# Kernel optimization log

Measured on AMD Instinct MI355X. Metric: run time of the kernel, lower is better.

## Reference

```python
import jax, jax.numpy as jnp
import numpy as np

B, T, D, H = 2, 2048, 1024, 16
DH = D // H  # 64


def setup_inputs() -> dict:
    key = jax.random.key(0)
    ks = jax.random.split(key, 8)
    s = 0.02  # typical init scale for projection weights
    return {
        "query_states": jax.random.normal(ks[0], (B, T, D), jnp.float32),
        "key_states": jax.random.normal(ks[1], (B, T, D), jnp.float32),
        "attention_mask": jnp.zeros((B, 1, 1, T), jnp.float32),
        "Wq": jax.random.normal(ks[2], (D, D), jnp.float32) * s,
        "bq": jnp.zeros((D,), jnp.float32),
        "Wk": jax.random.normal(ks[3], (D, D), jnp.float32) * s,
        "bk": jnp.zeros((D,), jnp.float32),
        "Wv": jax.random.normal(ks[4], (D, D), jnp.float32) * s,
        "bv": jnp.zeros((D,), jnp.float32),
        "mask_future": 0,
    }


def _heads(x):
    # [B, T, D] -> [B, H, T, DH]
    b, t, _ = x.shape
    return x.reshape(b, t, H, DH).transpose(0, 2, 1, 3)


def reference(query_states, key_states, attention_mask, Wq, bq, Wk, bk, Wv, bv, mask_future):
    q = _heads(query_states @ Wq + bq)   # [B,H,T,DH]
    k = _heads(key_states @ Wk + bk)     # [B,H,T,DH]
    v = _heads(key_states @ Wv + bv)     # [B,H,T,DH]
    scale = 1.0 / jnp.sqrt(jnp.asarray(DH, jnp.float32))
    scores = jnp.einsum("bhqd,bhkd->bhqk", q, k) * scale + attention_mask
    if mask_future:  # static Python int flag
        t = scores.shape[-1]
        triu = jnp.triu(jnp.ones((t, t), bool))  # includes diagonal, as in torch.triu
        scores = jnp.where(triu, -jnp.inf, scores)
    probs = jax.nn.softmax(scores, axis=-1)
    # dropout p=0.0 -> identity
    ctx = jnp.einsum("bhqk,bhkd->bhqd", probs, v)  # [B,H,T,DH]
    b, _, t, _ = ctx.shape
    return ctx.transpose(0, 2, 1, 3).reshape(b, t, H * DH)
```

## Files before the change

kernel.cpp:

```cpp
#include <hip/hip_runtime.h>

#define DEV __device__ __forceinline__

typedef _Float16 f16;
typedef __attribute__((ext_vector_type(2))) _Float16 f16x2;
typedef __attribute__((ext_vector_type(4))) _Float16 f16x4;
typedef __attribute__((ext_vector_type(8))) _Float16 f16x8;
typedef __attribute__((ext_vector_type(4))) float f32x4;
typedef __attribute__((ext_vector_type(16))) float f32x16;
typedef __attribute__((ext_vector_type(4))) int i32x4;

constexpr int B = 2, T = 2048, D = 1024, H = 16, DH = 64;
constexpr int M = B * T;
constexpr float LOG2E = 1.4426950408889634f;

DEV void gload_lds16(const void* g, void* l) {
  __builtin_amdgcn_global_load_lds(
      (const __attribute__((address_space(1))) void*)g,
      (__attribute__((address_space(3))) void*)l, 16, 0, 0);
}

DEV unsigned pack_pk(float a, float b) {
  auto v = __builtin_amdgcn_cvt_pkrtz(a, b);
  return __builtin_bit_cast(unsigned, v);
}

DEV float max3f(float a, float b, float c) { return fmaxf(fmaxf(a, b), c); }

#if __has_builtin(__builtin_amdgcn_permlane32_swap)
#define HAVE_PLSWAP 1
DEV void swap32(unsigned& a, unsigned& b) {
  auto r = __builtin_amdgcn_permlane32_swap((int)a, (int)b, false, false);
  a = (unsigned)r[0];
  b = (unsigned)r[1];
}
DEV float redmax32(float x) {
  unsigned a = __builtin_bit_cast(unsigned, x), b = a;
  swap32(a, b);
  return fmaxf(__builtin_bit_cast(float, a), __builtin_bit_cast(float, b));
}
DEV float redsum32(float x) {
  unsigned a = __builtin_bit_cast(unsigned, x), b = a;
  swap32(a, b);
  return __builtin_bit_cast(float, a) + __builtin_bit_cast(float, b);
}
#else
#define HAVE_PLSWAP 0
DEV float redmax32(float x) { return fmaxf(x, __shfl_xor(x, 32, 64)); }
DEV float redsum32(float x) { return x + __shfl_xor(x, 32, 64); }
#endif

__global__ __launch_bounds__(256) void cast_qk(
    const float* __restrict__ qin, const float* __restrict__ kin,
    f16* __restrict__ outq) {
  int bi = blockIdx.x;
  const float* in = (bi < 2048) ? qin : kin;
  f16* out = outq + ((bi < 2048) ? 0 : (size_t)M * D);
  int i = ((bi & 2047) * 256 + threadIdx.x) * 8;
  f32x4 a = *(const f32x4*)(in + i);
  f32x4 b = *(const f32x4*)(in + i + 4);
  f16x8 o;
  o[0] = (f16)a[0]; o[1] = (f16)a[1]; o[2] = (f16)a[2]; o[3] = (f16)a[3];
  o[4] = (f16)b[0]; o[5] = (f16)b[1]; o[6] = (f16)b[2]; o[7] = (f16)b[3];
  *(f16x8*)(out + i) = o;
}

__global__ __launch_bounds__(256) void transpose_cast(
    const float* __restrict__ Wq, const float* __restrict__ Wk,
    const float* __restrict__ Wv, f16* __restrict__ WT) {
  int mat = blockIdx.z;
  const float* W = (mat == 0) ? Wq : (mat == 1 ? Wk : Wv);
  f16* out = WT + (size_t)mat * D * D;
  __shared__ float tile[32][33];
  int nt = blockIdx.x * 32, kt = blockIdx.y * 32;
  int tx = threadIdx.x, ty = threadIdx.y;
  for (int j = 0; j < 4; ++j) {
    int r = ty + 8 * j;
    tile[r][tx] = W[(size_t)(kt + r) * D + nt + tx];
  }
  __syncthreads();
  for (int j = 0; j < 4; ++j) {
    int r = ty + 8 * j;
    out[(size_t)(nt + r) * D + kt + tx] = (f16)tile[tx][r];
  }
}

__global__ __launch_bounds__(256) void qkv_gemm(
    const f16* __restrict__ XQ, const f16* __restrict__ XK,
    const f16* __restrict__ WT, const float* __restrict__ bq,
    const float* __restrict__ bk, const float* __restrict__ bv,
    f16* __restrict__ QKV) {
  int mat = blockIdx.z;
  const f16* X = (mat == 0) ? XQ : XK;
  const f16* Wt = WT + (size_t)mat * D * D;
  const float* bias = (mat == 0) ? bq : (mat == 1 ? bk : bv);
  f16* out = QKV + (size_t)mat * M * D;
  float oscale = (mat == 0) ? 0.125f * LOG2E : 1.0f;
  int Lb = blockIdx.x + 8 * blockIdx.y;
  int n0 = (Lb & 7) * 128, m0 = (Lb >> 3) * 128;

  __shared__ f16 lds[2 * 2 * 128 * 64];
  char* lAb = (char*)lds;
  char* lBb = (char*)lds + 16384;

  int tid = threadIdx.x;
  int w = tid >> 6, lane = tid & 63;
  int l15 = lane & 15, lhi = lane >> 4;
  int wr = w >> 1, wc = w & 1;
  int r8 = lane >> 3, slot = lane & 7;
  int sslot = slot ^ r8;

  f32x4 acc[4][4] = {};
  constexpr int NKT = D / 64;

  auto STAGE = [&](int kt, int buf) {
#pragma unroll
    for (int i = 0; i < 4; ++i) {
      int chunk = w * 4 + i;
      int row = chunk * 8 + r8;
      gload_lds16(X + (size_t)(m0 + row) * D + kt * 64 + sslot * 8,
                  lAb + buf * 32768 + chunk * 1024);
      gload_lds16(Wt + (size_t)(n0 + row) * D + kt * 64 + sslot * 8,
                  lBb + buf * 32768 + chunk * 1024);
    }
  };

  STAGE(0, 0);
  __syncthreads();

  for (int kt = 0; kt < NKT; ++kt) {
    if (kt) __syncthreads();
    if (kt + 1 < NKT) STAGE(kt + 1, (kt + 1) & 1);
    const char* bA = lAb + (kt & 1) * 32768;
    const char* bB = lBb + (kt & 1) * 32768;
#pragma unroll
    for (int ks = 0; ks < 2; ++ks) {
      f16x8 aF[4], bF[4];
#pragma unroll
      for (int mt = 0; mt < 4; ++mt) {
        int row = wr * 64 + mt * 16 + l15;
        int byt = (row * 128 + ks * 64 + lhi * 16) ^ ((row & 7) << 4);
        aF[mt] = *(const f16x8*)(bA + byt);
      }
#pragma unroll
      for (int nt = 0; nt < 4; ++nt) {
        int row = wc * 64 + nt * 16 + l15;
        int byt = (row * 128 + ks * 64 + lhi * 16) ^ ((row & 7) << 4);
        bF[nt] = *(const f16x8*)(bB + byt);
      }
      __builtin_amdgcn_s_setprio(1);
#pragma unroll
      for (int mt = 0; mt < 4; ++mt)
#pragma unroll
        for (int nt = 0; nt < 4; ++nt)
          acc[mt][nt] = __builtin_amdgcn_mfma_f32_16x16x32_f16(
              aF[mt], bF[nt], acc[mt][nt], 0, 0, 0);
      __builtin_amdgcn_s_setprio(0);
    }
  }

  float bv4[4];
  for (int nt = 0; nt < 4; ++nt) bv4[nt] = bias[n0 + wc * 64 + nt * 16 + l15];
  if (mat < 2) {
    for (int mt = 0; mt < 4; ++mt)
      for (int nt = 0; nt < 4; ++nt) {
        int col = n0 + wc * 64 + nt * 16 + l15;
        int hh = col >> 6, dh = col & 63;
        for (int r = 0; r < 4; ++r) {
          int row = m0 + wr * 64 + mt * 16 + lhi * 4 + r;
          int bb = row >> 11, tt = row & (T - 1);
          out[((size_t)(bb * H + hh) * T + tt) * 64 + dh] =
              (f16)((acc[mt][nt][r] + bv4[nt]) * oscale);
        }
      }
  } else {
    for (int mt = 0; mt < 4; ++mt)
      for (int nt = 0; nt < 4; ++nt) {
        int col = n0 + wc * 64 + nt * 16 + l15;
        int hh = col >> 6, dh = col & 63;
        int row0 = m0 + wr * 64 + mt * 16 + lhi * 4;
        int bb = row0 >> 11, tt = row0 & (T - 1);
        f16x4 pk;
        for (int r = 0; r < 4; ++r) pk[r] = (f16)(acc[mt][nt][r] + bv4[nt]);
        *(f16x4*)(out + ((size_t)(bb * H + hh) * 64 + dh) * T + tt) = pk;
      }
  }
}

__global__ __launch_bounds__(256) void attn(
    const f16* __restrict__ QKV, const float* __restrict__ mask,
    const int* __restrict__ mfp, float* __restrict__ out) {
  int L = blockIdx.x + 16 * blockIdx.y + 256 * blockIdx.z;
  int e = L & 7, q = L >> 3;
  int bh = e * 4 + (q & 3);
  int q0 = (q >> 2) * 128;
  int b = bh >> 4, h = bh & 15;
  int mf = *mfp;
  constexpr int NT = T / 64;

  const f16* Qh = QKV + (size_t)bh * T * 64;
  const f16* Kh = QKV + (size_t)M * D + (size_t)bh * T * 64;
  const f16* VTh = QKV + (size_t)2 * M * D + (size_t)bh * 64 * T;

  __shared__ char smem[32768];

  int tid = threadIdx.x;
  int w = tid >> 6, lane = tid & 63;
  int l31 = lane & 31, hi = lane >> 5;
  int qrow = q0 + w * 32 + l31;

  const float* mb = mask + (size_t)b * T;
  bool lnz = false;
#pragma unroll
  for (int j = 0; j < 8; ++j) {
    f32x4 mv = *(const f32x4*)(mb + lane * 32 + j * 4);
    lnz |= (mv[0] != 0.f) | (mv[1] != 0.f) | (mv[2] != 0.f) | (mv[3] != 0.f);
  }
  int domask = __any(lnz) | mf;

  f16x8 qF[4];
  const f16* qp = Qh + (size_t)qrow * 64;
#pragma unroll
  for (int kc = 0; kc < 4; ++kc) qF[kc] = *(const f16x8*)(qp + kc * 16 + hi * 8);

  auto STAGE = [&](int kv0, int buf) {
    char* dK = smem + buf * 8192;
    char* dV = smem + 16384 + buf * 8192;
#pragma unroll
    for (int i = 0; i < 2; ++i) {
      int c = (w * 2 + i) * 64 + lane;
      int r = c >> 3;
      int slot = (c & 7) ^ (r & 7);
      gload_lds16(Kh + (size_t)(kv0 + r) * 64 + slot * 8, dK + (w * 2 + i) * 1024);
      gload_lds16(VTh + (size_t)r * T + kv0 + slot * 8, dV + (w * 2 + i) * 1024);
    }
  };

  float mprev = -1e30f, lsum = 0.f;
  f32x16 oAcc[2] = {};
  STAGE(0, 0);
  __syncthreads();

  for (int t = 0; t < NT; ++t) {
    if (t) __syncthreads();
    if (t + 1 < NT) STAGE((t + 1) * 64, (t + 1) & 1);
    int kv0 = t * 64;
    const char* bK = smem + (t & 1) * 8192;
    const char* bV = smem + 16384 + (t & 1) * 8192;

    f32x16 sA[2] = {};
    __builtin_amdgcn_s_setprio(1);
#pragma unroll
    for (int f = 0; f < 2; ++f)
#pragma unroll
      for (int kc = 0; kc < 4; ++kc) {
        int row = f * 32 + l31;
        f16x8 kF = *(const f16x8*)(bK + ((row * 128 + kc * 32 + hi * 16) ^ ((row & 7) << 4)));
        sA[f] = __builtin_amdgcn_mfma_f32_32x32x16_f16(kF, qF[kc], sA[f], 0, 0, 0);
      }
    __builtin_amdgcn_s_setprio(0);

    float mx;
    if (domask) {
      mx = -1e30f;
#pragma unroll
      for (int f = 0; f < 2; ++f)
#pragma unroll
        for (int r = 0; r < 16; ++r) {
          int kv = kv0 + f * 32 + (r & 3) + 8 * (r >> 2) + 4 * hi;
          float v = sA[f][r] + LOG2E * mb[kv];
          if (mf && kv >= qrow) v = -1e30f;
          sA[f][r] = v;
          mx = fmaxf(mx, v);
        }
    } else {
      float t0 = max3f(sA[0][0], sA[0][1], sA[0][2]);
      float t1 = max3f(sA[0][3], sA[0][4], sA[0][5]);
      float t2 = max3f(sA[0][6], sA[0][7], sA[0][8]);
      float t3 = max3f(sA[0][9], sA[0][10], sA[0][11]);
      float t4 = max3f(sA[0][12], sA[0][13], sA[0][14]);
      float t5 = max3f(sA[1][0], sA[1][1], sA[1][2]);
      float t6 = max3f(sA[1][3], sA[1][4], sA[1][5]);
      float t7 = max3f(sA[1][6], sA[1][7], sA[1][8]);
      float t8 = max3f(sA[1][9], sA[1][10], sA[1][11]);
      float t9 = max3f(sA[1][12], sA[1][13], sA[1][14]);
      float u0 = max3f(t0, t1, t2);
      float u1 = max3f(t3, t4, sA[0][15]);
      float u2 = max3f(t5, t6, t7);
      float u3 = max3f(t8, t9, sA[1][15]);
      mx = fmaxf(max3f(u0, u1, u2), u3);
    }
    mx = redmax32(mx);

    if (!__all(mx <= mprev + 8.f)) {
      float mn = fmaxf(mprev, mx);
      float asc = __builtin_amdgcn_exp2f(mprev - mn);
      lsum *= asc;
#pragma unroll
      for (int f = 0; f < 2; ++f)
#pragma unroll
        for (int r = 0; r < 16; ++r) oAcc[f][r] *= asc;
      mprev = mn;
    }

    float rs = 0.f;
#pragma unroll
    for (int f = 0; f < 2; ++f)
#pragma unroll
      for (int r = 0; r < 16; ++r) {
        float e2 = __builtin_amdgcn_exp2f(sA[f][r] - mprev);
        sA[f][r] = e2;
        rs += e2;
      }
    lsum += redsum32(rs);

    f16x8 pF[4];
#if HAVE_PLSWAP
#pragma unroll
    for (int f = 0; f < 2; ++f)
#pragma unroll
      for (int half = 0; half < 2; ++half) {
        unsigned p0 = pack_pk(sA[f][half * 8 + 0], sA[f][half * 8 + 1]);
        unsigned p1 = pack_pk(sA[f][half * 8 + 2], sA[f][half * 8 + 3]);
        unsigned p2 = pack_pk(sA[f][half * 8 + 4], sA[f][half * 8 + 5]);
        unsigned p3 = pack_pk(sA[f][half * 8 + 6], sA[f][half * 8 + 7]);
        swap32(p0, p2);
        swap32(p1, p3);
        i32x4 d;
        d[0] = (int)p0; d[1] = (int)p1; d[2] = (int)p2; d[3] = (int)p3;
        pF[f * 2 + half] = __builtin_bit_cast(f16x8, d);
      }
#else
#pragma unroll
    for (int f = 0; f < 2; ++f) {
      unsigned pk_[8], px_[8];
#pragma unroll
      for (int g = 0; g < 8; ++g) {
        pk_[g] = pack_pk(sA[f][2 * g], sA[f][2 * g + 1]);
        px_[g] = (unsigned)__shfl_xor((int)pk_[g], 32, 64);
      }
#pragma unroll
      for (int half = 0; half < 2; ++half) {
        int o = half * 4;
        i32x4 d;
        d[0] = (int)(hi ? px_[o + 2] : pk_[o + 0]);
        d[1] = (int)(hi ? px_[o + 3] : pk_[o + 1]);
        d[2] = (int)(hi ? pk_[o + 2] : px_[o + 0]);
        d[3] = (int)(hi ? pk_[o + 3] : px_[o + 1]);
        pF[f * 2 + half] = __builtin_bit_cast(f16x8, d);
      }
    }
#endif

    __builtin_amdgcn_s_setprio(1);
#pragma unroll
    for (int df = 0; df < 2; ++df)
#pragma unroll
      for (int kc = 0; kc < 4; ++kc) {
        int row = df * 32 + l31;
        f16x8 vF = *(const f16x8*)(bV + ((row * 128 + kc * 32 + hi * 16) ^ ((row & 7) << 4)));
        oAcc[df] = __builtin_amdgcn_mfma_f32_32x32x16_f16(vF, pF[kc], oAcc[df], 0, 0, 0);
      }
    __builtin_amdgcn_s_setprio(0);
  }

  __syncthreads();
  float linv = 1.0f / lsum;
  float* sOw = (float*)smem + w * 2048;
#pragma unroll
  for (int df = 0; df < 2; ++df)
#pragma unroll
    for (int r = 0; r < 16; ++r) {
      int d = df * 32 + 4 * hi + (r & 3) + 8 * (r >> 2);
      sOw[l31 * 64 + (d ^ l31)] = oAcc[df][r] * linv;
    }
  __syncthreads();
  float* op0 = out + (size_t)(b * T + q0 + w * 32) * D + h * 64;
#pragma unroll
  for (int r2 = 0; r2 < 32; ++r2) {
    float v = sOw[r2 * 64 + (lane ^ r2)];
    op0[(size_t)r2 * D + lane] = v;
  }
}

extern "C" void kernel_launch(void* const* d_in, const int* in_sizes, int n_in,
                              void* d_out, int out_size, void* d_ws, size_t ws_size,
                              hipStream_t stream) {
  const float* q_in = (const float*)d_in[0];
  const float* k_in = (const float*)d_in[1];
  const float* amask = (const float*)d_in[2];
  const float* Wq = (const float*)d_in[3];
  const float* bq = (const float*)d_in[4];
  const float* Wk = (const float*)d_in[5];
  const float* bk = (const float*)d_in[6];
  const float* Wv = (const float*)d_in[7];
  const float* bv = (const float*)d_in[8];
  const int* mf = (const int*)d_in[9];
  float* out = (float*)d_out;

  char* ws = (char*)d_ws;
  f16* XQK = (f16*)ws;
  f16* WT = (f16*)(ws + (((size_t)16) << 20));
  f16* QKV = (f16*)(ws + (((size_t)24) << 20));

  cast_qk<<<4096, 256, 0, stream>>>(q_in, k_in, XQK);
  transpose_cast<<<dim3(32, 32, 3), dim3(32, 8), 0, stream>>>(Wq, Wk, Wv, WT);
  qkv_gemm<<<dim3(8, 32, 3), 256, 0, stream>>>(XQK, XQK + (size_t)M * D, WT, bq,
                                               bk, bv, QKV);
  attn<<<dim3(16, 16, 2), 256, 0, stream>>>(QKV, amask, mf, out);
}
```

Measured before the change: 203.5 us.

## Merge prep kernels, single-buffer QKV GEMM, stage epilogue through LDS

Combines the input cast and weight transpose-cast into one launch to save a kernel launch. The QKV GEMM drops double-buffered LDS prefetch and setprio in favour of a single buffer with two barriers per k-step. Its epilogue now writes results to swizzled LDS and then emits coalesced 16-byte global stores for both the head-major Q/K layout and the transposed V layout. The attention softmax row sum is now a tree reduction over the exponentiated scores instead of a serial accumulation. Removing the prefetch exposes global load latency in the GEMM main loop, which may offset the cheaper epilogue.

Result: no change. 207.0 us (+1.7%).

```diff
diff --git a/kernel.cpp b/kernel.cpp
--- a/kernel.cpp
+++ b/kernel.cpp
@@ -27,6 +27,14 @@
 
 DEV float max3f(float a, float b, float c) { return fmaxf(fmaxf(a, b), c); }
 
+DEV float sum16(const f32x16& v) {
+  float a = (v[0] + v[1]) + (v[2] + v[3]);
+  float b = (v[4] + v[5]) + (v[6] + v[7]);
+  float c = (v[8] + v[9]) + (v[10] + v[11]);
+  float d = (v[12] + v[13]) + (v[14] + v[15]);
+  return (a + b) + (c + d);
+}
+
 #if __has_builtin(__builtin_amdgcn_permlane32_swap)
 #define HAVE_PLSWAP 1
 DEV void swap32(unsigned& a, unsigned& b) {
@@ -50,30 +58,33 @@
 DEV float redsum32(float x) { return x + __shfl_xor(x, 32, 64); }
 #endif
 
-__global__ __launch_bounds__(256) void cast_qk(
+__global__ __launch_bounds__(256) void prep(
     const float* __restrict__ qin, const float* __restrict__ kin,
-    f16* __restrict__ outq) {
+    const float* __restrict__ Wq, const float* __restrict__ Wk,
+    const float* __restrict__ Wv, f16* __restrict__ XQK,
+    f16* __restrict__ WT) {
   int bi = blockIdx.x;
-  const float* in = (bi < 2048) ? qin : kin;
-  f16* out = outq + ((bi < 2048) ? 0 : (size_t)M * D);
-  int i = ((bi & 2047) * 256 + threadIdx.x) * 8;
-  f32x4 a = *(const f32x4*)(in + i);
-  f32x4 b = *(const f32x4*)(in + i + 4);
-  f16x8 o;
-  o[0] = (f16)a[0]; o[1] = (f16)a[1]; o[2] = (f16)a[2]; o[3] = (f16)a[3];
-  o[4] = (f16)b[0]; o[5] = (f16)b[1]; o[6] = (f16)b[2]; o[7] = (f16)b[3];
-  *(f16x8*)(out + i) = o;
-}
-
-__global__ __launch_bounds__(256) void transpose_cast(
-    const float* __restrict__ Wq, const float* __restrict__ Wk,
-    const float* __restrict__ Wv, f16* __restrict__ WT) {
-  int mat = blockIdx.z;
+  int tid = threadIdx.x;
+  if (bi < 4096) {
+    const float* in = (bi < 2048) ? qin : kin;
+    f16* out = XQK + ((bi < 2048) ? 0 : (size_t)M * D);
+    int i = ((bi & 2047) * 256 + tid) * 8;
+    f32x4 a = *(const f32x4*)(in + i);
+    f32x4 b = *(const f32x4*)(in + i + 4);
+    f16x8 o;
+    o[0] = (f16)a[0]; o[1] = (f16)a[1]; o[2] = (f16)a[2]; o[3] = (f16)a[3];
+    o[4] = (f16)b[0]; o[5] = (f16)b[1]; o[6] = (f16)b[2]; o[7] = (f16)b[3];
+    *(f16x8*)(out + i) = o;
+    return;
+  }
+  int t = bi - 4096;
+  int mat = t >> 10;
+  int rem = t & 1023;
+  int nt = (rem & 31) * 32, kt = (rem >> 5) * 32;
   const float* W = (mat == 0) ? Wq : (mat == 1 ? Wk : Wv);
   f16* out = WT + (size_t)mat * D * D;
   __shared__ float tile[32][33];
-  int nt = blockIdx.x * 32, kt = blockIdx.y * 32;
-  int tx = threadIdx.x, ty = threadIdx.y;
+  int tx = tid & 31, ty = tid >> 5;
   for (int j = 0; j < 4; ++j) {
     int r = ty + 8 * j;
     tile[r][tx] = W[(size_t)(kt + r) * D + nt + tx];
@@ -99,7 +110,7 @@
   int Lb = blockIdx.x + 8 * blockIdx.y;
   int n0 = (Lb & 7) * 128, m0 = (Lb >> 3) * 128;
 
-  __shared__ f16 lds[2 * 2 * 128 * 64];
+  __shared__ f16 lds[2 * 128 * 64];
   char* lAb = (char*)lds;
   char* lBb = (char*)lds + 16384;
 
@@ -111,28 +122,19 @@
   int sslot = slot ^ r8;
 
   f32x4 acc[4][4] = {};
-  constexpr int NKT = D / 64;
-
-  auto STAGE = [&](int kt, int buf) {
+
+  for (int kt = 0; kt < D / 64; ++kt) {
+    __syncthreads();
 #pragma unroll
     for (int i = 0; i < 4; ++i) {
       int chunk = w * 4 + i;
       int row = chunk * 8 + r8;
       gload_lds16(X + (size_t)(m0 + row) * D + kt * 64 + sslot * 8,
-                  lAb + buf * 32768 + chunk * 1024);
+                  lAb + chunk * 1024);
       gload_lds16(Wt + (size_t)(n0 + row) * D + kt * 64 + sslot * 8,
-                  lBb + buf * 32768 + chunk * 1024);
-    }
-  };
-
-  STAGE(0, 0);
-  __syncthreads();
-
-  for (int kt = 0; kt < NKT; ++kt) {
-    if (kt) __syncthreads();
-    if (kt + 1 < NKT) STAGE(kt + 1, (kt + 1) & 1);
-    const char* bA = lAb + (kt & 1) * 32768;
-    const char* bB = lBb + (kt & 1) * 32768;
+                  lBb + chunk * 1024);
+    }
+    __syncthreads();
 #pragma unroll
     for (int ks = 0; ks < 2; ++ks) {
       f16x8 aF[4], bF[4];
@@ -140,50 +142,78 @@
       for (int mt = 0; mt < 4; ++mt) {
         int row = wr * 64 + mt * 16 + l15;
         int byt = (row * 128 + ks * 64 + lhi * 16) ^ ((row & 7) << 4);
-        aF[mt] = *(const f16x8*)(bA + byt);
+        aF[mt] = *(const f16x8*)(lAb + byt);
       }
 #pragma unroll
       for (int nt = 0; nt < 4; ++nt) {
         int row = wc * 64 + nt * 16 + l15;
         int byt = (row * 128 + ks * 64 + lhi * 16) ^ ((row & 7) << 4);
-        bF[nt] = *(const f16x8*)(bB + byt);
-      }
-      __builtin_amdgcn_s_setprio(1);
+        bF[nt] = *(const f16x8*)(lBb + byt);
+      }
 #pragma unroll
       for (int mt = 0; mt < 4; ++mt)
 #pragma unroll
         for (int nt = 0; nt < 4; ++nt)
           acc[mt][nt] = __builtin_amdgcn_mfma_f32_16x16x32_f16(
               aF[mt], bF[nt], acc[mt][nt], 0, 0, 0);
-      __builtin_amdgcn_s_setprio(0);
-    }
-  }
-
+    }
+  }
+
+  __syncthreads();
+  char* cb = lAb;
   float bv4[4];
+#pragma unroll
   for (int nt = 0; nt < 4; ++nt) bv4[nt] = bias[n0 + wc * 64 + nt * 16 + l15];
+
   if (mat < 2) {
+#pragma unroll
     for (int mt = 0; mt < 4; ++mt)
+#pragma unroll
       for (int nt = 0; nt < 4; ++nt) {
-        int col = n0 + wc * 64 + nt * 16 + l15;
-        int hh = col >> 6, dh = col & 63;
+        int col = wc * 64 + nt * 16 + l15;
+#pragma unroll
         for (int r = 0; r < 4; ++r) {
-          int row = m0 + wr * 64 + mt * 16 + lhi * 4 + r;
-          int bb = row >> 11, tt = row & (T - 1);
-          out[((size_t)(bb * H + hh) * T + tt) * 64 + dh] =
+          int row = wr * 64 + mt * 16 + lhi * 4 + r;
+          *(f16*)(cb + ((row * 256 + col * 2) ^ ((row & 7) << 4))) =
               (f16)((acc[mt][nt][r] + bv4[nt]) * oscale);
         }
       }
+    __syncthreads();
+    int bb = m0 >> 11, t0 = m0 & (T - 1);
+    int hh0 = (n0 >> 6);
+#pragma unroll
+    for (int p = 0; p < 8; ++p) {
+      int row = p * 16 + (tid >> 4);
+      int c = tid & 15;
+      f16x8 v = *(const f16x8*)(cb + row * 256 + ((c ^ (row & 7)) << 4));
+      int col0 = c * 8;
+      int hh = hh0 + (col0 >> 6), dh = col0 & 63;
+      *(f16x8*)(out + ((size_t)(bb * H + hh) * T + t0 + row) * 64 + dh) = v;
+    }
   } else {
+#pragma unroll
     for (int mt = 0; mt < 4; ++mt)
+#pragma unroll
       for (int nt = 0; nt < 4; ++nt) {
-        int col = n0 + wc * 64 + nt * 16 + l15;
-        int hh = col >> 6, dh = col & 63;
-        int row0 = m0 + wr * 64 + mt * 16 + lhi * 4;
-        int bb = row0 >> 11, tt = row0 & (T - 1);
-        f16x4 pk;
-        for (int r = 0; r < 4; ++r) pk[r] = (f16)(acc[mt][nt][r] + bv4[nt]);
-        *(f16x4*)(out + ((size_t)(bb * H + hh) * 64 + dh) * T + tt) = pk;
-      }
+        int col = wc * 64 + nt * 16 + l15;
+#pragma unroll
+        for (int r = 0; r < 4; ++r) {
+          int row = wr * 64 + mt * 16 + lhi * 4 + r;
+          *(f16*)(cb + ((col * 256 + row * 2) ^ ((col & 7) << 4))) =
+              (f16)(acc[mt][nt][r] + bv4[nt]);
+        }
+      }
+    __syncthreads();
+    int bb = m0 >> 11, t0 = m0 & (T - 1);
+    int hh0 = (n0 >> 6);
+#pragma unroll
+    for (int p = 0; p < 8; ++p) {
+      int col = p * 16 + (tid >> 4);
+      int c = tid & 15;
+      f16x8 v = *(const f16x8*)(cb + col * 256 + ((c ^ (col & 7)) << 4));
+      int hh = hh0 + (col >> 6), dh = col & 63;
+      *(f16x8*)(out + ((size_t)(bb * H + hh) * 64 + dh) * T + t0 + c * 8) = v;
+    }
   }
 }
 
@@ -303,16 +333,12 @@
       mprev = mn;
     }
 
-    float rs = 0.f;
 #pragma unroll
     for (int f = 0; f < 2; ++f)
 #pragma unroll
-      for (int r = 0; r < 16; ++r) {
-        float e2 = __builtin_amdgcn_exp2f(sA[f][r] - mprev);
-        sA[f][r] = e2;
-        rs += e2;
-      }
-    lsum += redsum32(rs);
+      for (int r = 0; r < 16; ++r)
+        sA[f][r] = __builtin_amdgcn_exp2f(sA[f][r] - mprev);
+    lsum += redsum32(sum16(sA[0]) + sum16(sA[1]));
 
     f16x8 pF[4];
 #if HAVE_PLSWAP
@@ -403,8 +429,7 @@
   f16* WT = (f16*)(ws + (((size_t)16) << 20));
   f16* QKV = (f16*)(ws + (((size_t)24) << 20));
 
-  cast_qk<<<4096, 256, 0, stream>>>(q_in, k_in, XQK);
-  transpose_cast<<<dim3(32, 32, 3), dim3(32, 8), 0, stream>>>(Wq, Wk, Wv, WT);
+  prep<<<7168, 256, 0, stream>>>(q_in, k_in, Wq, Wk, Wv, XQK, WT);
   qkv_gemm<<<dim3(8, 32, 3), 256, 0, stream>>>(XQK, XQK + (size_t)M * D, WT, bq,
                                                bk, bv, QKV);
   attn<<<dim3(16, 16, 2), 256, 0, stream>>>(QKV, amask, mf, out);
```
